# Performance work log

Measured on AMD Instinct MI355X. Metric: run time of the kernel, lower is better.

## Reference

```python
import jax, jax.numpy as jnp
import numpy as np

N_ELEMENTS = 64  # StructureElementLayer(n_elements=64)


def setup_inputs() -> dict:
    key = jax.random.key(0)
    k1, k2 = jax.random.split(key)
    # x: [N, C, T, V] skeleton sequence (batch, coord channels, time, joints)
    x = jax.random.normal(k1, (256, 3, 256, 25), dtype=jnp.float32)
    # StructureElementLayer parameters (torch.rand init / ones*3 init)
    centres = jax.random.uniform(k2, (N_ELEMENTS, 2), dtype=jnp.float32)
    sharpness = jnp.ones((N_ELEMENTS, 2), dtype=jnp.float32) * 3.0
    return {"x": x, "centres": centres, "sharpness": sharpness}


def _mst_deaths(D):
    """Dim-0 Vietoris-Rips persistence deaths == MST edge weights (Prim's algorithm).

    D: [n, n] symmetric distance matrix. Returns [n-1] finite death values
    (births are all 0; the single essential (0, inf) pair contributes
    exp(-inf)=0 to the structure-element layer and is dropped).
    """
    n = D.shape[0]
    in_tree = jnp.zeros((n,), dtype=bool).at[0].set(True)
    dist = D[0]  # min distance from each node to the current tree

    def step(carry, _):
        in_tree, dist = carry
        d = jnp.where(in_tree, jnp.inf, dist)
        j = jnp.argmin(d)
        w = d[j]
        in_tree = in_tree.at[j].set(True)
        dist = jnp.minimum(dist, D[j])
        return (in_tree, dist), w

    (_, _), deaths = jax.lax.scan(step, (in_tree, dist), None, length=n - 1)
    return deaths


def _forward(x, centres, sharpness):
    xm = x.mean(1)                                  # [N, T, V]
    diff = xm[..., :, None] - xm[..., None, :]      # [N, T, V, V] pairwise joint diffs
    diff = diff.mean(-3)                            # [N, V, V]
    feat = jnp.linalg.norm(diff, axis=1)            # [N, V]  (torch.norm(., 2, dim=1))
    feat = (feat - feat.min()) / (feat.max() - feat.min())
    # Euclidean distance matrix of the N points in V-dim space (grad-safe sqrt)
    sq = jnp.sum(feat * feat, axis=1)
    D2 = sq[:, None] + sq[None, :] - 2.0 * (feat @ feat.T)
    D2 = jnp.maximum(D2, 0.0)
    D = jnp.where(D2 > 0.0, jnp.sqrt(jnp.where(D2 > 0.0, D2, 1.0)), 0.0)
    deaths = _mst_deaths(D)                         # [N-1]
    diag = jnp.stack([jnp.zeros_like(deaths), deaths], axis=-1)  # [N-1, 2] (birth, death)
    # StructureElementLayer: sum_i exp(-sum_d (p_id - c_kd)^2 * s_kd^2)
    d2 = (diag[:, None, :] - centres[None, :, :]) ** 2            # [N-1, K, 2]
    out = jnp.exp(-(d2 * (sharpness ** 2)).sum(-1)).sum(0)        # [K]
    return out


def reference(x, centres, sharpness):
    return _forward(x, centres, sharpness)
```

## Files before the change

kernel.cpp:

```cpp
#include <hip/hip_runtime.h>
#include <hip/hip_fp16.h>


#define WS_FEAT 0
#define WS_FMN  26624
#define WS_FMX  27648
#define WS_RK   28672
#define WS_D16  65536

#define INF32 0xFFFFFFFFu
#define SA 132
#define SB 68
#define OFF_B (128 * SA)

__global__ void __launch_bounds__(256) k_feat(const float* __restrict__ x,
                                              float* __restrict__ featG,
                                              float* __restrict__ fmnG,
                                              float* __restrict__ fmxG) {
    __shared__ float sums[25];
    __shared__ float mrow[25];
    __shared__ float S12[2];
    __shared__ unsigned int bmn, bmx;
    const int n = blockIdx.x;
    const int tid = threadIdx.x;
    if (tid < 25) sums[tid] = 0.0f;
    if (tid == 0) { bmn = 0x7F800000u; bmx = 0u; }
    __syncthreads();
    if (tid < 200) {
        const float* base = x + (long)n * 19200 + 4 * tid;
        float a0 = 0.f, a1 = 0.f, a2 = 0.f, a3 = 0.f;
        #pragma unroll
        for (int i = 0; i < 24; ++i) {
            float4 v = *reinterpret_cast<const float4*>(base + 800 * i);
            a0 += v.x; a1 += v.y; a2 += v.z; a3 += v.w;
        }
        const int v0 = (4 * tid) % 25;
        atomicAdd(&sums[v0], a0);
        atomicAdd(&sums[(v0 + 1) % 25], a1);
        atomicAdd(&sums[(v0 + 2) % 25], a2);
        atomicAdd(&sums[(v0 + 3) % 25], a3);
    }
    __syncthreads();
    if (tid < 25) mrow[tid] = sums[tid] * (1.0f / 768.0f);
    __syncthreads();
    if (tid == 0) {
        float S1 = 0.f, S2 = 0.f;
        #pragma unroll
        for (int v = 0; v < 25; ++v) { S1 += mrow[v]; S2 += mrow[v] * mrow[v]; }
        S12[0] = S1; S12[1] = S2;
    }
    __syncthreads();
    if (tid < 25) {
        const float r = mrow[tid];
        float q = S12[1] - 2.f * r * S12[0] + 25.f * r * r;
        q = fmaxf(q, 0.f);
        const float f = sqrtf(q);
        featG[n * 26 + tid] = f;
        atomicMin(&bmn, __float_as_uint(f));
        atomicMax(&bmx, __float_as_uint(f));
    }
    __syncthreads();
    if (tid == 0) { fmnG[n] = __uint_as_float(bmn); fmxG[n] = __uint_as_float(bmx); }
}

template <int CTRL>
__device__ __forceinline__ unsigned int dpp_min_step(unsigned int v) {
    unsigned int t = (unsigned int)__builtin_amdgcn_update_dpp(
        (int)0xFFFFFFFF, (int)v, CTRL, 0xF, 0xF, false);
    return (t < v) ? t : v;
}

__global__ void __launch_bounds__(256) k_dist(const float* __restrict__ featG,
                                              unsigned short* __restrict__ D16,
                                              unsigned int* __restrict__ rowKeyG) {
    __shared__ float featS[6656];
    __shared__ unsigned int wred[4];
    const int i = blockIdx.x;
    const int t = threadIdx.x;
    #pragma unroll
    for (int it = 0; it < 7; ++it) {
        const int o = it * 256 + t;
        if (o < 1664) reinterpret_cast<float4*>(featS)[o] =
            reinterpret_cast<const float4*>(featG)[o];
    }
    __syncthreads();
    float fi[25];
    #pragma unroll
    for (int v = 0; v < 25; ++v) fi[v] = featS[i * 26 + v];
    float s = 0.f;
    #pragma unroll
    for (int v = 0; v < 25; ++v) {
        const float d = fi[v] - featS[t * 26 + v];
        s += d * d;
    }
    const unsigned int w16 = (unsigned int)__half_as_ushort(__float2half(s));
    D16[i * 256 + t] = (unsigned short)w16;
    const unsigned int lo = (t < i) ? t : i, hi = (t < i) ? i : t;
    unsigned int key = (t == i) ? INF32 : ((w16 << 16) | (lo << 8) | hi);
    key = dpp_min_step<0x111>(key);
    key = dpp_min_step<0x112>(key);
    key = dpp_min_step<0x114>(key);
    key = dpp_min_step<0x118>(key);
    key = dpp_min_step<0x142>(key);
    key = dpp_min_step<0x143>(key);
    if ((t & 63) == 63) wred[t >> 6] = key;
    __syncthreads();
    if (t == 0) {
        const unsigned int b0 = wred[0] < wred[1] ? wred[0] : wred[1];
        const unsigned int b1 = wred[2] < wred[3] ? wred[2] : wred[3];
        rowKeyG[i] = b0 < b1 ? b0 : b1;
    }
}

template <bool RECORD>
__device__ __forceinline__ unsigned int wave0_phase(int n, int lane,
        unsigned int* rowKeyS, unsigned char* parentS, unsigned char* newidS,
        unsigned char* cmapS, float* deaths, unsigned int* ncS, unsigned int* dcS) {
    unsigned int par[4];
    #pragma unroll
    for (int s = 0; s < 4; ++s) {
        const int i = lane + 64 * s;
        if (i < n) {
            const unsigned int rk = rowKeyS[i];
            const unsigned int u = (rk >> 8) & 0xFFu, v = rk & 0xFFu;
            unsigned int p = (u == (unsigned int)i) ? v : u;
            if (rk == INF32) p = (unsigned int)i;
            par[s] = p;
            parentS[i] = (unsigned char)p;
        }
    }
    #pragma unroll
    for (int s = 0; s < 4; ++s) {
        const int i = lane + 64 * s;
        if (i < n) {
            const unsigned int p = par[s];
            if (p != (unsigned int)i) {
                if (parentS[p] == (unsigned char)i && (unsigned int)i < p) {
                    parentS[i] = (unsigned char)i;
                } else if (RECORD) {
                    const unsigned int d = atomicAdd(dcS, 1u);
                    const unsigned int rk = rowKeyS[i];
                    deaths[d] = sqrtf(__half2float(__ushort_as_half(
                        (unsigned short)(rk >> 16))));
                }
            }
        }
    }
    for (;;) {
        bool ch = false;
        #pragma unroll
        for (int s = 0; s < 4; ++s) {
            const int i = lane + 64 * s;
            if (i < n) {
                const unsigned char p0 = parentS[i];
                const unsigned char np = parentS[p0];
                if (np != p0) { ch = true; parentS[i] = np; }
            }
        }
        if (__ballot(ch) == 0ull) break;
    }
    bool isr[4];
    #pragma unroll
    for (int s = 0; s < 4; ++s) {
        const int i = lane + 64 * s;
        isr[s] = (i < n) && (parentS[i] == (unsigned char)i);
    }
    unsigned int base = 0;
    const unsigned long long below = (1ull << lane) - 1ull;
    #pragma unroll
    for (int s = 0; s < 4; ++s) {
        const unsigned long long mask = __ballot(isr[s]);
        if (isr[s]) {
            const int i = lane + 64 * s;
            newidS[i] = (unsigned char)(base + __popcll(mask & below));
        }
        base += (unsigned int)__popcll(mask);
    }
    if (lane == 0) *ncS = base;
    #pragma unroll
    for (int s = 0; s < 4; ++s) {
        const int i = lane + 64 * s;
        if (i < n) cmapS[i] = newidS[parentS[i]];
    }
    return base;
}

__global__ void __launch_bounds__(1024) k_mst(const unsigned short* __restrict__ D16g,
                                              const unsigned int* __restrict__ rowKeyG,
                                              const float* __restrict__ fmnG,
                                              const float* __restrict__ fmxG,
                                              const float* __restrict__ centres,
                                              const float* __restrict__ sharp,
                                              float* __restrict__ out) {
    __shared__ unsigned int Mb[128 * SA + 64 * SB];
    __shared__ unsigned int rowKeyS[256];
    __shared__ unsigned char parentS[256], newidS[256], cmapS[256];
    __shared__ unsigned int ncS, dcS;
    __shared__ float deathsS[256];
    __shared__ unsigned int mmS[2];
    __shared__ float outpart[1024];
    const int tid = threadIdx.x;
    const int wv = tid >> 6, lane = tid & 63;

    if (tid < 256) rowKeyS[tid] = rowKeyG[tid];
    if (tid == 0) { dcS = 0; mmS[0] = 0x7F800000u; mmS[1] = 0u; }
    __syncthreads();

    if (wv == 0) {
        wave0_phase<true>(256, lane, rowKeyS, parentS, newidS, cmapS,
                          deathsS, &ncS, &dcS);
    } else if (wv == 15) {
        #pragma unroll
        for (int q = 0; q < 4; ++q) {
            const int j = (tid - 960) * 4 + q;
            atomicMin(&mmS[0], __float_as_uint(fmnG[j]));
            atomicMax(&mmS[1], __float_as_uint(fmxG[j]));
        }
    } else {
        for (int w = tid - 64; w < 128 * SA; w += 896) Mb[w] = INF32;
    }
    __syncthreads();

    {
        const unsigned int* D32 = reinterpret_cast<const unsigned int*>(D16g);
        for (int u = tid; u < 32768; u += 1024) {
            const unsigned int w = D32[u];
            const int r = u >> 7;
            const int c = (u & 127) << 1;
            const unsigned int ca = cmapS[r];
            const unsigned int e0 = w & 0xFFFFu;
            const unsigned int e1 = w >> 16;
            const unsigned int cb0 = cmapS[c];
            const unsigned int cb1 = cmapS[c + 1];
            if (ca != cb0) {
                const unsigned int lo = ca < cb0 ? ca : cb0;
                const unsigned int hi = ca < cb0 ? cb0 : ca;
                atomicMin(&Mb[ca * SA + cb0], (e0 << 16) | (lo << 8) | hi);
            }
            if (ca != cb1) {
                const unsigned int lo = ca < cb1 ? ca : cb1;
                const unsigned int hi = ca < cb1 ? cb1 : ca;
                atomicMin(&Mb[ca * SA + cb1], (e1 << 16) | (lo << 8) | hi);
            }
        }
    }
    __syncthreads();

    if (wv == 0) {
        int n = (int)ncS;
        int srcOff = 0, srcStr = SA, dstOff = OFF_B, dstStr = SB;
        for (int round = 0; round < 12 && n > 1; ++round) {
            for (int a = lane; a < n; a += 64) {
                const unsigned int* row = &Mb[srcOff + a * srcStr];
                unsigned int best = INF32;
                for (int b2 = 0; b2 < n; ++b2) {
                    const unsigned int v = row[b2];
                    best = v < best ? v : best;
                }
                rowKeyS[a] = best;
            }
            __builtin_amdgcn_wave_barrier();
            const unsigned int nc = wave0_phase<true>(n, lane, rowKeyS, parentS,
                                                      newidS, cmapS, deathsS,
                                                      &ncS, &dcS);
            __builtin_amdgcn_wave_barrier();
            if (nc > 1) {
                for (int w = lane; w < (int)nc * dstStr; w += 64)
                    Mb[dstOff + w] = INF32;
                __builtin_amdgcn_wave_barrier();
                for (int a = lane; a < n; a += 64) {
                    const unsigned int ca = cmapS[a];
                    const unsigned int* row = &Mb[srcOff + a * srcStr];
                    for (int b2 = 0; b2 < n; ++b2) {
                        const unsigned int cb = cmapS[b2];
                        const unsigned int v = row[b2];
                        if (ca != cb && v != INF32) {
                            const unsigned int lo = ca < cb ? ca : cb;
                            const unsigned int hi = ca < cb ? cb : ca;
                            atomicMin(&Mb[dstOff + ca * dstStr + cb],
                                      (v & 0xFFFF0000u) | (lo << 8) | hi);
                        }
                    }
                }
                __builtin_amdgcn_wave_barrier();
            }
            const int t1 = srcOff; srcOff = dstOff; dstOff = t1;
            const int t2 = srcStr; srcStr = dstStr; dstStr = t2;
            n = (int)nc;
        }
    }
    __syncthreads();

    const float mn = __uint_as_float(mmS[0]);
    const float mx = __uint_as_float(mmS[1]);
    const float inv = 1.0f / (mx - mn);
    const int k = tid & 63;
    const int part = tid >> 6;
    const float c0 = centres[2 * k], c1 = centres[2 * k + 1];
    const float s0 = sharp[2 * k],   s1 = sharp[2 * k + 1];
    const float t0 = c0 * c0 * s0 * s0;
    const float s1sq = s1 * s1;
    float acc = 0.f;
    for (int idx = part; idx < 255; idx += 16) {
        const float d = deathsS[idx] * inv - c1;
        acc += __expf(-(t0 + d * d * s1sq));
    }
    outpart[tid] = acc;
    __syncthreads();
    if (tid < 64) {
        float s = 0.f;
        #pragma unroll
        for (int pp = 0; pp < 16; ++pp) s += outpart[tid + 64 * pp];
        out[tid] = s;
    }
}

extern "C" void kernel_launch(void* const* d_in, const int* in_sizes, int n_in,
                              void* d_out, int out_size, void* d_ws, size_t ws_size,
                              hipStream_t stream) {
    const float* x       = (const float*)d_in[0];
    const float* centres = (const float*)d_in[1];
    const float* sharp   = (const float*)d_in[2];
    float* out = (float*)d_out;
    char* ws = (char*)d_ws;
    float*          featG = (float*)(ws + WS_FEAT);
    float*          fmnG  = (float*)(ws + WS_FMN);
    float*          fmxG  = (float*)(ws + WS_FMX);
    unsigned int*   rk    = (unsigned int*)(ws + WS_RK);
    unsigned short* D16   = (unsigned short*)(ws + WS_D16);

    k_feat<<<256, 256, 0, stream>>>(x, featG, fmnG, fmxG);
    k_dist<<<256, 256, 0, stream>>>(featG, D16, rk);
    k_mst<<<1, 1024, 0, stream>>>(D16, rk, fmnG, fmxG, centres, sharp, out);
}
```

Measured before the change: 112.5 us.

## Split first Boruvka contraction into multi-block kernel and finish MST with Prim

Moves the first Boruvka contraction (component labeling plus building the contracted min-edge matrix) out of the single-block MST kernel into a new 256-block kernel. Each block recomputes the component map and scatters one row of D16 into a global matrix that k_feat pre-initialises to INF. The single-block kernel then loads the contracted matrix and runs a wave-level Prim's algorithm using DPP min reductions, replacing the repeated Boruvka rounds. This adds an extra kernel launch and global atomics in exchange for removing serial single-block work over the 256x256 matrix.

```diff
diff --git a/kernel.cpp b/kernel.cpp
--- a/kernel.cpp
+++ b/kernel.cpp
@@ -6,23 +6,26 @@
 #define WS_FMN  26624
 #define WS_FMX  27648
 #define WS_RK   28672
+#define WS_DTH  29696
+#define WS_NCDC 30720
 #define WS_D16  65536
+#define WS_MP   196608
 
 #define INF32 0xFFFFFFFFu
 #define SA 132
-#define SB 68
-#define OFF_B (128 * SA)
 
 __global__ void __launch_bounds__(256) k_feat(const float* __restrict__ x,
                                               float* __restrict__ featG,
                                               float* __restrict__ fmnG,
-                                              float* __restrict__ fmxG) {
+                                              float* __restrict__ fmxG,
+                                              unsigned int* __restrict__ Mp) {
     __shared__ float sums[25];
     __shared__ float mrow[25];
     __shared__ float S12[2];
     __shared__ unsigned int bmn, bmx;
     const int n = blockIdx.x;
     const int tid = threadIdx.x;
+    if (tid < 66) Mp[n * 66 + tid] = INF32;
     if (tid < 25) sums[tid] = 0.0f;
     if (tid == 0) { bmn = 0x7F800000u; bmx = 0u; }
     __syncthreads();
@@ -113,7 +116,7 @@
 }
 
 template <bool RECORD>
-__device__ __forceinline__ unsigned int wave0_phase(int n, int lane,
+__device__ __forceinline__ void wave0_phase(int n, int lane,
         unsigned int* rowKeyS, unsigned char* parentS, unsigned char* newidS,
         unsigned char* cmapS, float* deaths, unsigned int* ncS, unsigned int* dcS) {
     unsigned int par[4];
@@ -182,111 +185,109 @@
         const int i = lane + 64 * s;
         if (i < n) cmapS[i] = newidS[parentS[i]];
     }
-    return base;
-}
-
-__global__ void __launch_bounds__(1024) k_mst(const unsigned short* __restrict__ D16g,
-                                              const unsigned int* __restrict__ rowKeyG,
+}
+
+__global__ void __launch_bounds__(256) k_contract(const unsigned short* __restrict__ D16g,
+                                                  const unsigned int* __restrict__ rowKeyG,
+                                                  unsigned int* __restrict__ Mp,
+                                                  float* __restrict__ deathsG,
+                                                  unsigned int* __restrict__ ncdcG) {
+    __shared__ unsigned int rowKeyS[256];
+    __shared__ unsigned char parentS[256], newidS[256], cmapS[256];
+    __shared__ unsigned int ncS, dcS;
+    __shared__ float deathsS[256];
+    const int tid = threadIdx.x;
+    const int b = blockIdx.x;
+    rowKeyS[tid] = rowKeyG[tid];
+    if (tid == 0) dcS = 0;
+    __syncthreads();
+    if (tid < 64) {
+        if (b == 0)
+            wave0_phase<true>(256, tid, rowKeyS, parentS, newidS, cmapS,
+                              deathsS, &ncS, &dcS);
+        else
+            wave0_phase<false>(256, tid, rowKeyS, parentS, newidS, cmapS,
+                               nullptr, &ncS, nullptr);
+    }
+    __syncthreads();
+    if (b == 0) {
+        if (tid < dcS) deathsG[tid] = deathsS[tid];
+        if (tid == 0) { ncdcG[0] = ncS; ncdcG[1] = dcS; }
+    }
+    const unsigned int ca = cmapS[b];
+    const unsigned int cb = cmapS[tid];
+    if (ca != cb) {
+        const unsigned int w16 = (unsigned int)D16g[b * 256 + tid];
+        const unsigned int lo = ca < cb ? ca : cb;
+        const unsigned int hi = ca < cb ? cb : ca;
+        atomicMin(&Mp[ca * SA + cb], (w16 << 16) | (lo << 8) | hi);
+    }
+}
+
+__global__ void __launch_bounds__(1024) k_mst(const unsigned int* __restrict__ Mp,
+                                              const float* __restrict__ deathsG,
+                                              const unsigned int* __restrict__ ncdcG,
                                               const float* __restrict__ fmnG,
                                               const float* __restrict__ fmxG,
                                               const float* __restrict__ centres,
                                               const float* __restrict__ sharp,
                                               float* __restrict__ out) {
-    __shared__ unsigned int Mb[128 * SA + 64 * SB];
-    __shared__ unsigned int rowKeyS[256];
-    __shared__ unsigned char parentS[256], newidS[256], cmapS[256];
-    __shared__ unsigned int ncS, dcS;
+    __shared__ unsigned int Mb[128 * SA];
     __shared__ float deathsS[256];
     __shared__ unsigned int mmS[2];
     __shared__ float outpart[1024];
+    __shared__ unsigned int ncS, dcS;
     const int tid = threadIdx.x;
     const int wv = tid >> 6, lane = tid & 63;
 
-    if (tid < 256) rowKeyS[tid] = rowKeyG[tid];
-    if (tid == 0) { dcS = 0; mmS[0] = 0x7F800000u; mmS[1] = 0u; }
-    __syncthreads();
-
-    if (wv == 0) {
-        wave0_phase<true>(256, lane, rowKeyS, parentS, newidS, cmapS,
-                          deathsS, &ncS, &dcS);
-    } else if (wv == 15) {
+    if (tid == 0) {
+        ncS = ncdcG[0]; dcS = ncdcG[1];
+        mmS[0] = 0x7F800000u; mmS[1] = 0u;
+    }
+    if (tid < 256) deathsS[tid] = deathsG[tid];
+    __syncthreads();
+    const int nc = (int)ncS;
+    for (int idx = tid; idx < nc * SA; idx += 1024) Mb[idx] = Mp[idx];
+    if (wv == 15) {
         #pragma unroll
         for (int q = 0; q < 4; ++q) {
-            const int j = (tid - 960) * 4 + q;
+            const int j = lane * 4 + q;
             atomicMin(&mmS[0], __float_as_uint(fmnG[j]));
             atomicMax(&mmS[1], __float_as_uint(fmxG[j]));
         }
-    } else {
-        for (int w = tid - 64; w < 128 * SA; w += 896) Mb[w] = INF32;
-    }
-    __syncthreads();
-
-    {
-        const unsigned int* D32 = reinterpret_cast<const unsigned int*>(D16g);
-        for (int u = tid; u < 32768; u += 1024) {
-            const unsigned int w = D32[u];
-            const int r = u >> 7;
-            const int c = (u & 127) << 1;
-            const unsigned int ca = cmapS[r];
-            const unsigned int e0 = w & 0xFFFFu;
-            const unsigned int e1 = w >> 16;
-            const unsigned int cb0 = cmapS[c];
-            const unsigned int cb1 = cmapS[c + 1];
-            if (ca != cb0) {
-                const unsigned int lo = ca < cb0 ? ca : cb0;
-                const unsigned int hi = ca < cb0 ? cb0 : ca;
-                atomicMin(&Mb[ca * SA + cb0], (e0 << 16) | (lo << 8) | hi);
+    }
+    __syncthreads();
+
+    if (wv == 0) {
+        const int dc = (int)dcS;
+        unsigned int d0 = (Mb[lane]      & 0xFFFF0000u) | (unsigned)lane;
+        unsigned int d1 = (Mb[64 + lane] & 0xFFFF0000u) | (unsigned)(64 + lane);
+        unsigned int tb = 0;
+        if (lane == 0) { tb = 1u; d0 = INF32; }
+        for (int it = 0; it < nc - 1; ++it) {
+            unsigned int key = d0 < d1 ? d0 : d1;
+            key = dpp_min_step<0x111>(key);
+            key = dpp_min_step<0x112>(key);
+            key = dpp_min_step<0x114>(key);
+            key = dpp_min_step<0x118>(key);
+            key = dpp_min_step<0x142>(key);
+            key = dpp_min_step<0x143>(key);
+            const unsigned int best =
+                (unsigned int)__builtin_amdgcn_readlane((int)key, 63);
+            const unsigned int j = best & 0xFFu;
+            if (lane == 0)
+                deathsS[dc + it] = sqrtf(__half2float(__ushort_as_half(
+                    (unsigned short)(best >> 16))));
+            const unsigned int lj = j & 63u, slot = j >> 6;
+            if ((unsigned)lane == lj) {
+                tb |= (1u << slot);
+                if (slot == 0u) d0 = INF32; else d1 = INF32;
             }
-            if (ca != cb1) {
-                const unsigned int lo = ca < cb1 ? ca : cb1;
-                const unsigned int hi = ca < cb1 ? cb1 : ca;
-                atomicMin(&Mb[ca * SA + cb1], (e1 << 16) | (lo << 8) | hi);
-            }
-        }
-    }
-    __syncthreads();
-
-    if (wv == 0) {
-        int n = (int)ncS;
-        int srcOff = 0, srcStr = SA, dstOff = OFF_B, dstStr = SB;
-        for (int round = 0; round < 12 && n > 1; ++round) {
-            for (int a = lane; a < n; a += 64) {
-                const unsigned int* row = &Mb[srcOff + a * srcStr];
-                unsigned int best = INF32;
-                for (int b2 = 0; b2 < n; ++b2) {
-                    const unsigned int v = row[b2];
-                    best = v < best ? v : best;
-                }
-                rowKeyS[a] = best;
-            }
-            __builtin_amdgcn_wave_barrier();
-            const unsigned int nc = wave0_phase<true>(n, lane, rowKeyS, parentS,
-                                                      newidS, cmapS, deathsS,
-                                                      &ncS, &dcS);
-            __builtin_amdgcn_wave_barrier();
-            if (nc > 1) {
-                for (int w = lane; w < (int)nc * dstStr; w += 64)
-                    Mb[dstOff + w] = INF32;
-                __builtin_amdgcn_wave_barrier();
-                for (int a = lane; a < n; a += 64) {
-                    const unsigned int ca = cmapS[a];
-                    const unsigned int* row = &Mb[srcOff + a * srcStr];
-                    for (int b2 = 0; b2 < n; ++b2) {
-                        const unsigned int cb = cmapS[b2];
-                        const unsigned int v = row[b2];
-                        if (ca != cb && v != INF32) {
-                            const unsigned int lo = ca < cb ? ca : cb;
-                            const unsigned int hi = ca < cb ? cb : ca;
-                            atomicMin(&Mb[dstOff + ca * dstStr + cb],
-                                      (v & 0xFFFF0000u) | (lo << 8) | hi);
-                        }
-                    }
-                }
-                __builtin_amdgcn_wave_barrier();
-            }
-            const int t1 = srcOff; srcOff = dstOff; dstOff = t1;
-            const int t2 = srcStr; srcStr = dstStr; dstStr = t2;
-            n = (int)nc;
+            const unsigned int rb = j * SA;
+            const unsigned int n0 = (Mb[rb + lane]      & 0xFFFF0000u) | (unsigned)lane;
+            const unsigned int n1 = (Mb[rb + 64 + lane] & 0xFFFF0000u) | (unsigned)(64 + lane);
+            d0 = (tb & 1u) ? INF32 : (n0 < d0 ? n0 : d0);
+            d1 = (tb & 2u) ? INF32 : (n1 < d1 ? n1 : d1);
         }
     }
     __syncthreads();
@@ -327,9 +328,13 @@
     float*          fmnG  = (float*)(ws + WS_FMN);
     float*          fmxG  = (float*)(ws + WS_FMX);
     unsigned int*   rk    = (unsigned int*)(ws + WS_RK);
+    float*          dth   = (float*)(ws + WS_DTH);
+    unsigned int*   ncdc  = (unsigned int*)(ws + WS_NCDC);
     unsigned short* D16   = (unsigned short*)(ws + WS_D16);
-
-    k_feat<<<256, 256, 0, stream>>>(x, featG, fmnG, fmxG);
+    unsigned int*   Mp    = (unsigned int*)(ws + WS_MP);
+
+    k_feat<<<256, 256, 0, stream>>>(x, featG, fmnG, fmxG, Mp);
     k_dist<<<256, 256, 0, stream>>>(featG, D16, rk);
-    k_mst<<<1, 1024, 0, stream>>>(D16, rk, fmnG, fmxG, centres, sharp, out);
-}
+    k_contract<<<256, 256, 0, stream>>>(D16, rk, Mp, dth, ncdc);
+    k_mst<<<1, 1024, 0, stream>>>(Mp, dth, ncdc, fmnG, fmxG, centres, sharp, out);
+}
```

New measurement: 112.9 us. About the same (+0.4%).
